# Kernel tuning notes

Hardware: AMD Instinct MI355X
Metric: run time of the kernel (lower is better)

The kernel has to match this reference:

```python
import jax, jax.numpy as jnp
import numpy as np

# Fixed causal graph: 32 endo nodes, each with a private 16-dim exogenous parent.
# Nodes 0..3 are roots (no endo parents); node i>=4 has endo parents {i-4..i-1}.
N_NODES = 32
ENDO = 16      # endogenous features per node
EXO = 16       # exogenous features per node
HID = 64       # hidden width (module default hidden_features=[64,64])
N_ROOTS = 4
N_PAR = 4      # endo parents for non-root nodes
IN_ROOT = EXO                      # 16
IN_INNER = N_PAR * ENDO + EXO      # 80
BATCH = 32768


def _init(key, shape, fan_in):
    return jax.random.normal(key, shape, jnp.float32) * (1.0 / np.sqrt(fan_in))


def setup_inputs() -> dict:
    key = jax.random.key(0)
    ks = jax.random.split(key, 13)
    n_in = N_NODES - N_ROOTS
    return {
        "u": jax.random.normal(ks[0], (BATCH, N_NODES * EXO), jnp.float32),
        # stacked root MLPs: [n_roots, in, out]
        "w_r1": _init(ks[1], (N_ROOTS, IN_ROOT, HID), IN_ROOT),
        "b_r1": jnp.zeros((N_ROOTS, HID), jnp.float32),
        "w_r2": _init(ks[2], (N_ROOTS, HID, HID), HID),
        "b_r2": jnp.zeros((N_ROOTS, HID), jnp.float32),
        "w_r3": _init(ks[3], (N_ROOTS, HID, ENDO), HID),
        "b_r3": jnp.zeros((N_ROOTS, ENDO), jnp.float32),
        # stacked inner MLPs: [n_inner, in, out]
        "w_i1": _init(ks[4], (n_in, IN_INNER, HID), IN_INNER),
        "b_i1": jnp.zeros((n_in, HID), jnp.float32),
        "w_i2": _init(ks[5], (n_in, HID, HID), HID),
        "b_i2": jnp.zeros((n_in, HID), jnp.float32),
        "w_i3": _init(ks[6], (n_in, HID, ENDO), HID),
        "b_i3": jnp.zeros((n_in, ENDO), jnp.float32),
    }


def _mlp(x, w1, b1, w2, b2, w3, b3):
    h = jax.nn.relu(x @ w1 + b1)
    h = jax.nn.relu(h @ w2 + b2)
    return h @ w3 + b3


def reference(u, w_r1, b_r1, w_r2, b_r2, w_r3, b_r3,
              w_i1, b_i1, w_i2, b_i2, w_i3, b_i3):
    B = u.shape[0]
    U = u.reshape(B, N_NODES, EXO)  # per-node exogenous inputs
    # Root nodes: no endo parents, vectorized over the 4 roots.
    h = jax.nn.relu(jnp.einsum("bni,nio->bno", U[:, :N_ROOTS], w_r1) + b_r1)
    h = jax.nn.relu(jnp.einsum("bnh,nho->bno", h, w_r2) + b_r2)
    root_v = jnp.einsum("bnh,nhd->bnd", h, w_r3) + b_r3  # [B, 4, ENDO]
    V = [root_v[:, i] for i in range(N_ROOTS)]
    # Non-root nodes in topological order: gather thresholded parents -> MLP.
    for i in range(N_ROOTS, N_NODES):
        j = i - N_ROOTS
        parents = jnp.concatenate(
            [(V[p] > 0.5).astype(u.dtype) for p in range(i - N_PAR, i)], axis=-1)
        inp = jnp.concatenate([parents, U[:, i]], axis=-1)  # [B, 80]
        V.append(_mlp(inp, w_i1[j], b_i1[j], w_i2[j], b_i2[j], w_i3[j], b_i3[j]))
    # forward() uses soft=True, T/W_T/W_E=None -> E is the raw logits, batched.
    return jnp.concatenate(V, axis=-1)  # [B, N_NODES*ENDO]
```

## Files before the change

kernel.cpp:

```cpp
#include <hip/hip_runtime.h>


#define BT 64

typedef __attribute__((ext_vector_type(8))) short bf16x8;
typedef __attribute__((ext_vector_type(4))) float f32x4;
#define MFMA16 __builtin_amdgcn_mfma_f32_16x16x32_bf16

#define NODE_STRIDE 33792
#define W1_SPLIT    6144
#define W2_OFF      18432
#define W2_SPLIT    4096
#define W3_OFF      30720
#define W3_SPLIT    1024

__device__ inline unsigned short bf16_rne(float x) {
    unsigned u = __float_as_uint(x);
    u += 0x7fffu + ((u >> 16) & 1u);
    return (unsigned short)(u >> 16);
}
__device__ inline float bf16_tof(unsigned short h) {
    return __uint_as_float(((unsigned)h) << 16);
}
__device__ inline void split3(float x, unsigned short& h, unsigned short& m,
                              unsigned short& l) {
    h = bf16_rne(x);
    float r = x - bf16_tof(h);
    m = bf16_rne(r);
    float r2 = r - bf16_tof(m);
    l = bf16_rne(r2);
}

#define PER_NODE_ITEMS (64 * 96 + 64 * 64 + 16 * 64)

__global__ void prep_weights(const float* __restrict__ w_r1,
                             const float* __restrict__ w_r2,
                             const float* __restrict__ w_r3,
                             const float* __restrict__ w_i1,
                             const float* __restrict__ w_i2,
                             const float* __restrict__ w_i3,
                             unsigned short* __restrict__ ws) {
    int tid = blockIdx.x * 256 + threadIdx.x;
    if (tid >= 32 * PER_NODE_ITEMS) return;
    int node = tid / PER_NODE_ITEMS;
    int r = tid - node * PER_NODE_ITEMS;
    int off, stride;
    float wv = 0.0f;
    if (r < 6144) {
        int n = r / 96, k = r - n * 96;
        if (k < 64) {
            wv = (node >= 4) ? w_i1[((node - 4) * 80 + k) * 64 + n] : 0.0f;
        } else if (k < 80) {
            wv = (node < 4) ? w_r1[(node * 16 + (k - 64)) * 64 + n]
                            : w_i1[((node - 4) * 80 + k) * 64 + n];
        }
        off = n * 96 + k; stride = W1_SPLIT;
    } else if (r < 10240) {
        int r2 = r - 6144;
        int n = r2 >> 6, k = r2 & 63;
        wv = (node < 4) ? w_r2[(node * 64 + k) * 64 + n]
                        : w_i2[((node - 4) * 64 + k) * 64 + n];
        off = W2_OFF + n * 64 + k; stride = W2_SPLIT;
    } else {
        int r3 = r - 10240;
        int n = r3 >> 6, k = r3 & 63;
        wv = (node < 4) ? w_r3[(node * 64 + k) * 16 + n]
                        : w_i3[((node - 4) * 64 + k) * 16 + n];
        off = W3_OFF + n * 64 + k; stride = W3_SPLIT;
    }
    unsigned short h, m, l;
    split3(wv, h, m, l);
    unsigned short* base = ws + node * NODE_STRIDE;
    base[off] = h;
    base[off + stride] = m;
    base[off + 2 * stride] = l;
}

__global__ __launch_bounds__(256, 2) void ncm_mfma(
    const float* __restrict__ u,
    const unsigned short* __restrict__ ws,
    const float* __restrict__ b_r1, const float* __restrict__ b_r2,
    const float* __restrict__ b_r3, const float* __restrict__ b_i1,
    const float* __restrict__ b_i2, const float* __restrict__ b_i3,
    float* __restrict__ out)
{
    __shared__ __align__(16) unsigned short ring[4][64][24];
    __shared__ __align__(16) unsigned short xu[3][64][32];
    __shared__ __align__(16) unsigned short h1s[3][64][72];
    __shared__ __align__(16) unsigned short h2s[3][64][72];

    const int tid = threadIdx.x;
    const int l   = tid & 63;
    const int w   = tid >> 6;
    const int lr  = l & 15;
    const int lq  = l >> 4;

    for (int z = tid; z < 4 * 64 * 24; z += 256) ((unsigned short*)ring)[z] = 0;
    for (int z = tid; z < 3 * 64 * 32; z += 256) ((unsigned short*)xu)[z] = 0;

    const long eg = (long)blockIdx.x * BT;
    const float* u_blk = u + eg * 512;
    const int n1 = 16 * w + lr;

    for (int i = 0; i < 32; ++i) {
        __syncthreads();

        float4 uv = *(const float4*)(u_blk + (long)l * 512 + i * 16 + w * 4);
        {
            unsigned short h0, m0, l0, h1, m1, l1, h2, m2, l2, h3, m3, l3;
            split3(uv.x, h0, m0, l0); split3(uv.y, h1, m1, l1);
            split3(uv.z, h2, m2, l2); split3(uv.w, h3, m3, l3);
            ushort4 vh = make_ushort4(h0, h1, h2, h3);
            ushort4 vm = make_ushort4(m0, m1, m2, m3);
            ushort4 vl = make_ushort4(l0, l1, l2, l3);
            *(ushort4*)&xu[0][l][4 * w] = vh;
            *(ushort4*)&xu[1][l][4 * w] = vm;
            *(ushort4*)&xu[2][l][4 * w] = vl;
        }
        __syncthreads();

        const unsigned short* Wn = ws + i * NODE_STRIDE;

        f32x4 acc[4] = {{0,0,0,0},{0,0,0,0},{0,0,0,0},{0,0,0,0}};
        {
            if (i >= 4) {
                #pragma unroll
                for (int k0 = 0; k0 < 64; k0 += 32) {
                    const int f = k0 + lq * 8;
                    const int slot = (i + (f >> 4)) & 3;
                    bf16x8 wb0 = *(const bf16x8*)(Wn + 0 * W1_SPLIT + n1 * 96 + f);
                    bf16x8 wb1 = *(const bf16x8*)(Wn + 1 * W1_SPLIT + n1 * 96 + f);
                    bf16x8 wb2 = *(const bf16x8*)(Wn + 2 * W1_SPLIT + n1 * 96 + f);
                    #pragma unroll
                    for (int m = 0; m < 4; ++m) {
                        bf16x8 ab = *(const bf16x8*)&ring[slot][m * 16 + lr][f & 15];
                        acc[m] = MFMA16(ab, wb0, acc[m], 0, 0, 0);
                        acc[m] = MFMA16(ab, wb1, acc[m], 0, 0, 0);
                        acc[m] = MFMA16(ab, wb2, acc[m], 0, 0, 0);
                    }
                }
            }
            {
                const int f = lq * 8;
                bf16x8 wb0 = *(const bf16x8*)(Wn + 0 * W1_SPLIT + n1 * 96 + 64 + f);
                bf16x8 wb1 = *(const bf16x8*)(Wn + 1 * W1_SPLIT + n1 * 96 + 64 + f);
                bf16x8 wb2 = *(const bf16x8*)(Wn + 2 * W1_SPLIT + n1 * 96 + 64 + f);
                #pragma unroll
                for (int m = 0; m < 4; ++m) {
                    const int e = m * 16 + lr;
                    bf16x8 a0 = *(const bf16x8*)&xu[0][e][f];
                    bf16x8 a1 = *(const bf16x8*)&xu[1][e][f];
                    bf16x8 a2 = *(const bf16x8*)&xu[2][e][f];
                    acc[m] = MFMA16(a0, wb0, acc[m], 0, 0, 0);
                    acc[m] = MFMA16(a0, wb1, acc[m], 0, 0, 0);
                    acc[m] = MFMA16(a0, wb2, acc[m], 0, 0, 0);
                    acc[m] = MFMA16(a1, wb0, acc[m], 0, 0, 0);
                    acc[m] = MFMA16(a1, wb1, acc[m], 0, 0, 0);
                    acc[m] = MFMA16(a1, wb2, acc[m], 0, 0, 0);
                    acc[m] = MFMA16(a2, wb0, acc[m], 0, 0, 0);
                    acc[m] = MFMA16(a2, wb1, acc[m], 0, 0, 0);
                }
            }
            const float b1 = (i < 4) ? b_r1[i * 64 + n1] : b_i1[(i - 4) * 64 + n1];
            #pragma unroll
            for (int m = 0; m < 4; ++m) {
                #pragma unroll
                for (int r = 0; r < 4; ++r) {
                    const int e = m * 16 + lq * 4 + r;
                    float v = fmaxf(acc[m][r] + b1, 0.0f);
                    unsigned short sh, sm, sl;
                    split3(v, sh, sm, sl);
                    h1s[0][e][n1] = sh; h1s[1][e][n1] = sm; h1s[2][e][n1] = sl;
                }
            }
        }
        __syncthreads();

        {
            #pragma unroll
            for (int m = 0; m < 4; ++m) acc[m] = (f32x4){0,0,0,0};
            const unsigned short* W2 = Wn + W2_OFF;
            #pragma unroll
            for (int k0 = 0; k0 < 64; k0 += 32) {
                const int f = k0 + lq * 8;
                bf16x8 wb0 = *(const bf16x8*)(W2 + 0 * W2_SPLIT + n1 * 64 + f);
                bf16x8 wb1 = *(const bf16x8*)(W2 + 1 * W2_SPLIT + n1 * 64 + f);
                bf16x8 wb2 = *(const bf16x8*)(W2 + 2 * W2_SPLIT + n1 * 64 + f);
                #pragma unroll
                for (int m = 0; m < 4; ++m) {
                    const int e = m * 16 + lr;
                    bf16x8 a0 = *(const bf16x8*)&h1s[0][e][f];
                    bf16x8 a1 = *(const bf16x8*)&h1s[1][e][f];
                    bf16x8 a2 = *(const bf16x8*)&h1s[2][e][f];
                    acc[m] = MFMA16(a0, wb0, acc[m], 0, 0, 0);
                    acc[m] = MFMA16(a0, wb1, acc[m], 0, 0, 0);
                    acc[m] = MFMA16(a0, wb2, acc[m], 0, 0, 0);
                    acc[m] = MFMA16(a1, wb0, acc[m], 0, 0, 0);
                    acc[m] = MFMA16(a1, wb1, acc[m], 0, 0, 0);
                    acc[m] = MFMA16(a1, wb2, acc[m], 0, 0, 0);
                    acc[m] = MFMA16(a2, wb0, acc[m], 0, 0, 0);
                    acc[m] = MFMA16(a2, wb1, acc[m], 0, 0, 0);
                }
            }
            const float b2 = (i < 4) ? b_r2[i * 64 + n1] : b_i2[(i - 4) * 64 + n1];
            #pragma unroll
            for (int m = 0; m < 4; ++m) {
                #pragma unroll
                for (int r = 0; r < 4; ++r) {
                    const int e = m * 16 + lq * 4 + r;
                    float v = fmaxf(acc[m][r] + b2, 0.0f);
                    unsigned short sh, sm, sl;
                    split3(v, sh, sm, sl);
                    h2s[0][e][n1] = sh; h2s[1][e][n1] = sm; h2s[2][e][n1] = sl;
                }
            }
        }
        __syncthreads();

        {
            f32x4 c3 = {0,0,0,0};
            const unsigned short* W3 = Wn + W3_OFF;
            #pragma unroll
            for (int k0 = 0; k0 < 64; k0 += 32) {
                const int f = k0 + lq * 8;
                bf16x8 wb0 = *(const bf16x8*)(W3 + 0 * W3_SPLIT + lr * 64 + f);
                bf16x8 wb1 = *(const bf16x8*)(W3 + 1 * W3_SPLIT + lr * 64 + f);
                bf16x8 wb2 = *(const bf16x8*)(W3 + 2 * W3_SPLIT + lr * 64 + f);
                const int e = 16 * w + lr;
                bf16x8 a0 = *(const bf16x8*)&h2s[0][e][f];
                bf16x8 a1 = *(const bf16x8*)&h2s[1][e][f];
                bf16x8 a2 = *(const bf16x8*)&h2s[2][e][f];
                c3 = MFMA16(a0, wb0, c3, 0, 0, 0);
                c3 = MFMA16(a0, wb1, c3, 0, 0, 0);
                c3 = MFMA16(a0, wb2, c3, 0, 0, 0);
                c3 = MFMA16(a1, wb0, c3, 0, 0, 0);
                c3 = MFMA16(a1, wb1, c3, 0, 0, 0);
                c3 = MFMA16(a1, wb2, c3, 0, 0, 0);
                c3 = MFMA16(a2, wb0, c3, 0, 0, 0);
                c3 = MFMA16(a2, wb1, c3, 0, 0, 0);
            }
            const float b3 = (i < 4) ? b_r3[i * 16 + lr] : b_i3[(i - 4) * 16 + lr];
            const int slot = i & 3;
            #pragma unroll
            for (int r = 0; r < 4; ++r) {
                const int e = 16 * w + lq * 4 + r;
                float v = c3[r] + b3;
                out[(eg + e) * 512 + i * 16 + lr] = v;
                ring[slot][e][lr] = (v > 0.5f) ? (unsigned short)0x3F80 : (unsigned short)0;
            }
        }
    }
}

extern "C" void kernel_launch(void* const* d_in, const int* in_sizes, int n_in,
                              void* d_out, int out_size, void* d_ws, size_t ws_size,
                              hipStream_t stream) {
    const float* u    = (const float*)d_in[0];
    const float* w_r1 = (const float*)d_in[1];
    const float* b_r1 = (const float*)d_in[2];
    const float* w_r2 = (const float*)d_in[3];
    const float* b_r2 = (const float*)d_in[4];
    const float* w_r3 = (const float*)d_in[5];
    const float* b_r3 = (const float*)d_in[6];
    const float* w_i1 = (const float*)d_in[7];
    const float* b_i1 = (const float*)d_in[8];
    const float* w_i2 = (const float*)d_in[9];
    const float* b_i2 = (const float*)d_in[10];
    const float* w_i3 = (const float*)d_in[11];
    const float* b_i3 = (const float*)d_in[12];
    float* out = (float*)d_out;
    unsigned short* ws = (unsigned short*)d_ws;

    prep_weights<<<dim3((32 * PER_NODE_ITEMS) / 256), dim3(256), 0, stream>>>(
        w_r1, w_r2, w_r3, w_i1, w_i2, w_i3, ws);

    ncm_mfma<<<dim3(512), dim3(256), 0, stream>>>(
        u, ws, b_r1, b_r2, b_r3, b_i1, b_i2, b_i3, out);
}
```

Measured before the change: 335.6 us.

## Give each wave its own 16-row batch slice to drop block barriers

Work is redistributed so each wave owns 16 batch rows end to end for all 32 nodes, with per-wave shared buffers. Block-wide __syncthreads become wave barriers. Operands are swapped so MFMA outputs are feature-major per row, which enables vectorized bias loads, ushort4 stores and float4 output writes. The cost is that each wave now loads the full weight set itself, so weight traffic from L1/L2 per wave rises about fourfold.

```diff
diff --git a/kernel.cpp b/kernel.cpp
--- a/kernel.cpp
+++ b/kernel.cpp
@@ -84,10 +84,10 @@
     const float* __restrict__ b_i2, const float* __restrict__ b_i3,
     float* __restrict__ out)
 {
-    __shared__ __align__(16) unsigned short ring[4][64][24];
-    __shared__ __align__(16) unsigned short xu[3][64][32];
-    __shared__ __align__(16) unsigned short h1s[3][64][72];
-    __shared__ __align__(16) unsigned short h2s[3][64][72];
+    __shared__ __align__(16) unsigned short ring[4][4][16][24];
+    __shared__ __align__(16) unsigned short xu[4][3][16][32];
+    __shared__ __align__(16) unsigned short h1s[4][3][16][72];
+    __shared__ __align__(16) unsigned short h2s[4][3][16][72];
 
     const int tid = threadIdx.x;
     const int l   = tid & 63;
@@ -95,160 +95,174 @@
     const int lr  = l & 15;
     const int lq  = l >> 4;
 
-    for (int z = tid; z < 4 * 64 * 24; z += 256) ((unsigned short*)ring)[z] = 0;
-    for (int z = tid; z < 3 * 64 * 32; z += 256) ((unsigned short*)xu)[z] = 0;
-
-    const long eg = (long)blockIdx.x * BT;
-    const float* u_blk = u + eg * 512;
-    const int n1 = 16 * w + lr;
+    for (int z = l; z < 4 * 16 * 24; z += 64) ((unsigned short*)ring[w])[z] = 0;
+    for (int z = l; z < 3 * 16 * 32; z += 64) ((unsigned short*)xu[w])[z] = 0;
+    __builtin_amdgcn_wave_barrier();
+
+    const long eg   = (long)blockIdx.x * BT;
+    const long erow = eg + w * 16 + lr;
+    const float* u_row   = u   + erow * 512;
+    float*       out_row = out + erow * 512;
 
     for (int i = 0; i < 32; ++i) {
-        __syncthreads();
-
-        float4 uv = *(const float4*)(u_blk + (long)l * 512 + i * 16 + w * 4);
-        {
+        const unsigned short* Wn = ws + i * NODE_STRIDE;
+
+        {
+            float4 uv = *(const float4*)(u_row + i * 16 + lq * 4);
             unsigned short h0, m0, l0, h1, m1, l1, h2, m2, l2, h3, m3, l3;
             split3(uv.x, h0, m0, l0); split3(uv.y, h1, m1, l1);
             split3(uv.z, h2, m2, l2); split3(uv.w, h3, m3, l3);
-            ushort4 vh = make_ushort4(h0, h1, h2, h3);
-            ushort4 vm = make_ushort4(m0, m1, m2, m3);
-            ushort4 vl = make_ushort4(l0, l1, l2, l3);
-            *(ushort4*)&xu[0][l][4 * w] = vh;
-            *(ushort4*)&xu[1][l][4 * w] = vm;
-            *(ushort4*)&xu[2][l][4 * w] = vl;
-        }
-        __syncthreads();
-
-        const unsigned short* Wn = ws + i * NODE_STRIDE;
+            *(ushort4*)&xu[w][0][lr][lq * 4] = make_ushort4(h0, h1, h2, h3);
+            *(ushort4*)&xu[w][1][lr][lq * 4] = make_ushort4(m0, m1, m2, m3);
+            *(ushort4*)&xu[w][2][lr][lq * 4] = make_ushort4(l0, l1, l2, l3);
+        }
+        __builtin_amdgcn_wave_barrier();
 
         f32x4 acc[4] = {{0,0,0,0},{0,0,0,0},{0,0,0,0},{0,0,0,0}};
-        {
-            if (i >= 4) {
-                #pragma unroll
-                for (int k0 = 0; k0 < 64; k0 += 32) {
-                    const int f = k0 + lq * 8;
-                    const int slot = (i + (f >> 4)) & 3;
-                    bf16x8 wb0 = *(const bf16x8*)(Wn + 0 * W1_SPLIT + n1 * 96 + f);
-                    bf16x8 wb1 = *(const bf16x8*)(Wn + 1 * W1_SPLIT + n1 * 96 + f);
-                    bf16x8 wb2 = *(const bf16x8*)(Wn + 2 * W1_SPLIT + n1 * 96 + f);
-                    #pragma unroll
-                    for (int m = 0; m < 4; ++m) {
-                        bf16x8 ab = *(const bf16x8*)&ring[slot][m * 16 + lr][f & 15];
-                        acc[m] = MFMA16(ab, wb0, acc[m], 0, 0, 0);
-                        acc[m] = MFMA16(ab, wb1, acc[m], 0, 0, 0);
-                        acc[m] = MFMA16(ab, wb2, acc[m], 0, 0, 0);
-                    }
-                }
-            }
-            {
-                const int f = lq * 8;
-                bf16x8 wb0 = *(const bf16x8*)(Wn + 0 * W1_SPLIT + n1 * 96 + 64 + f);
-                bf16x8 wb1 = *(const bf16x8*)(Wn + 1 * W1_SPLIT + n1 * 96 + 64 + f);
-                bf16x8 wb2 = *(const bf16x8*)(Wn + 2 * W1_SPLIT + n1 * 96 + 64 + f);
-                #pragma unroll
-                for (int m = 0; m < 4; ++m) {
-                    const int e = m * 16 + lr;
-                    bf16x8 a0 = *(const bf16x8*)&xu[0][e][f];
-                    bf16x8 a1 = *(const bf16x8*)&xu[1][e][f];
-                    bf16x8 a2 = *(const bf16x8*)&xu[2][e][f];
-                    acc[m] = MFMA16(a0, wb0, acc[m], 0, 0, 0);
-                    acc[m] = MFMA16(a0, wb1, acc[m], 0, 0, 0);
-                    acc[m] = MFMA16(a0, wb2, acc[m], 0, 0, 0);
-                    acc[m] = MFMA16(a1, wb0, acc[m], 0, 0, 0);
-                    acc[m] = MFMA16(a1, wb1, acc[m], 0, 0, 0);
-                    acc[m] = MFMA16(a1, wb2, acc[m], 0, 0, 0);
-                    acc[m] = MFMA16(a2, wb0, acc[m], 0, 0, 0);
-                    acc[m] = MFMA16(a2, wb1, acc[m], 0, 0, 0);
-                }
-            }
-            const float b1 = (i < 4) ? b_r1[i * 64 + n1] : b_i1[(i - 4) * 64 + n1];
-            #pragma unroll
-            for (int m = 0; m < 4; ++m) {
-                #pragma unroll
-                for (int r = 0; r < 4; ++r) {
-                    const int e = m * 16 + lq * 4 + r;
-                    float v = fmaxf(acc[m][r] + b1, 0.0f);
-                    unsigned short sh, sm, sl;
-                    split3(v, sh, sm, sl);
-                    h1s[0][e][n1] = sh; h1s[1][e][n1] = sm; h1s[2][e][n1] = sl;
-                }
-            }
-        }
-        __syncthreads();
-
-        {
-            #pragma unroll
-            for (int m = 0; m < 4; ++m) acc[m] = (f32x4){0,0,0,0};
-            const unsigned short* W2 = Wn + W2_OFF;
+
+        if (i >= 4) {
             #pragma unroll
             for (int k0 = 0; k0 < 64; k0 += 32) {
                 const int f = k0 + lq * 8;
-                bf16x8 wb0 = *(const bf16x8*)(W2 + 0 * W2_SPLIT + n1 * 64 + f);
-                bf16x8 wb1 = *(const bf16x8*)(W2 + 1 * W2_SPLIT + n1 * 64 + f);
-                bf16x8 wb2 = *(const bf16x8*)(W2 + 2 * W2_SPLIT + n1 * 64 + f);
+                const int slot = (i + (f >> 4)) & 3;
+                bf16x8 ab = *(const bf16x8*)&ring[w][slot][lr][f & 15];
                 #pragma unroll
-                for (int m = 0; m < 4; ++m) {
-                    const int e = m * 16 + lr;
-                    bf16x8 a0 = *(const bf16x8*)&h1s[0][e][f];
-                    bf16x8 a1 = *(const bf16x8*)&h1s[1][e][f];
-                    bf16x8 a2 = *(const bf16x8*)&h1s[2][e][f];
-                    acc[m] = MFMA16(a0, wb0, acc[m], 0, 0, 0);
-                    acc[m] = MFMA16(a0, wb1, acc[m], 0, 0, 0);
-                    acc[m] = MFMA16(a0, wb2, acc[m], 0, 0, 0);
-                    acc[m] = MFMA16(a1, wb0, acc[m], 0, 0, 0);
-                    acc[m] = MFMA16(a1, wb1, acc[m], 0, 0, 0);
-                    acc[m] = MFMA16(a1, wb2, acc[m], 0, 0, 0);
-                    acc[m] = MFMA16(a2, wb0, acc[m], 0, 0, 0);
-                    acc[m] = MFMA16(a2, wb1, acc[m], 0, 0, 0);
+                for (int ft = 0; ft < 4; ++ft) {
+                    const unsigned short* wp = Wn + (ft * 16 + lr) * 96 + f;
+                    bf16x8 wb0 = *(const bf16x8*)(wp);
+                    bf16x8 wb1 = *(const bf16x8*)(wp + W1_SPLIT);
+                    bf16x8 wb2 = *(const bf16x8*)(wp + 2 * W1_SPLIT);
+                    acc[ft] = MFMA16(wb0, ab, acc[ft], 0, 0, 0);
+                    acc[ft] = MFMA16(wb1, ab, acc[ft], 0, 0, 0);
+                    acc[ft] = MFMA16(wb2, ab, acc[ft], 0, 0, 0);
                 }
             }
-            const float b2 = (i < 4) ? b_r2[i * 64 + n1] : b_i2[(i - 4) * 64 + n1];
-            #pragma unroll
-            for (int m = 0; m < 4; ++m) {
-                #pragma unroll
-                for (int r = 0; r < 4; ++r) {
-                    const int e = m * 16 + lq * 4 + r;
-                    float v = fmaxf(acc[m][r] + b2, 0.0f);
-                    unsigned short sh, sm, sl;
-                    split3(v, sh, sm, sl);
-                    h2s[0][e][n1] = sh; h2s[1][e][n1] = sm; h2s[2][e][n1] = sl;
-                }
-            }
-        }
-        __syncthreads();
-
-        {
-            f32x4 c3 = {0,0,0,0};
-            const unsigned short* W3 = Wn + W3_OFF;
+        }
+        {
+            const int f = lq * 8;
+            bf16x8 a0 = *(const bf16x8*)&xu[w][0][lr][f];
+            bf16x8 a1 = *(const bf16x8*)&xu[w][1][lr][f];
+            bf16x8 a2 = *(const bf16x8*)&xu[w][2][lr][f];
+            #pragma unroll
+            for (int ft = 0; ft < 4; ++ft) {
+                const unsigned short* wp = Wn + (ft * 16 + lr) * 96 + 64 + f;
+                bf16x8 wb0 = *(const bf16x8*)(wp);
+                bf16x8 wb1 = *(const bf16x8*)(wp + W1_SPLIT);
+                bf16x8 wb2 = *(const bf16x8*)(wp + 2 * W1_SPLIT);
+                acc[ft] = MFMA16(wb0, a0, acc[ft], 0, 0, 0);
+                acc[ft] = MFMA16(wb1, a0, acc[ft], 0, 0, 0);
+                acc[ft] = MFMA16(wb2, a0, acc[ft], 0, 0, 0);
+                acc[ft] = MFMA16(wb0, a1, acc[ft], 0, 0, 0);
+                acc[ft] = MFMA16(wb1, a1, acc[ft], 0, 0, 0);
+                acc[ft] = MFMA16(wb2, a1, acc[ft], 0, 0, 0);
+                acc[ft] = MFMA16(wb0, a2, acc[ft], 0, 0, 0);
+                acc[ft] = MFMA16(wb1, a2, acc[ft], 0, 0, 0);
+            }
+        }
+        {
+            const float* B1 = (i < 4) ? (b_r1 + i * 64) : (b_i1 + (i - 4) * 64);
+            #pragma unroll
+            for (int ft = 0; ft < 4; ++ft) {
+                float4 bv = *(const float4*)(B1 + ft * 16 + lq * 4);
+                float v0 = fmaxf(acc[ft][0] + bv.x, 0.0f);
+                float v1 = fmaxf(acc[ft][1] + bv.y, 0.0f);
+                float v2 = fmaxf(acc[ft][2] + bv.z, 0.0f);
+                float v3 = fmaxf(acc[ft][3] + bv.w, 0.0f);
+                unsigned short h0, m0, l0, h1, m1, l1, h2, m2, l2, h3, m3, l3;
+                split3(v0, h0, m0, l0); split3(v1, h1, m1, l1);
+                split3(v2, h2, m2, l2); split3(v3, h3, m3, l3);
+                const int o = ft * 16 + lq * 4;
+                *(ushort4*)&h1s[w][0][lr][o] = make_ushort4(h0, h1, h2, h3);
+                *(ushort4*)&h1s[w][1][lr][o] = make_ushort4(m0, m1, m2, m3);
+                *(ushort4*)&h1s[w][2][lr][o] = make_ushort4(l0, l1, l2, l3);
+            }
+        }
+        __builtin_amdgcn_wave_barrier();
+
+        #pragma unroll
+        for (int ft = 0; ft < 4; ++ft) acc[ft] = (f32x4){0, 0, 0, 0};
+        {
+            const unsigned short* W2 = Wn + W2_OFF;
             #pragma unroll
             for (int k0 = 0; k0 < 64; k0 += 32) {
                 const int f = k0 + lq * 8;
-                bf16x8 wb0 = *(const bf16x8*)(W3 + 0 * W3_SPLIT + lr * 64 + f);
-                bf16x8 wb1 = *(const bf16x8*)(W3 + 1 * W3_SPLIT + lr * 64 + f);
-                bf16x8 wb2 = *(const bf16x8*)(W3 + 2 * W3_SPLIT + lr * 64 + f);
-                const int e = 16 * w + lr;
-                bf16x8 a0 = *(const bf16x8*)&h2s[0][e][f];
-                bf16x8 a1 = *(const bf16x8*)&h2s[1][e][f];
-                bf16x8 a2 = *(const bf16x8*)&h2s[2][e][f];
-                c3 = MFMA16(a0, wb0, c3, 0, 0, 0);
-                c3 = MFMA16(a0, wb1, c3, 0, 0, 0);
-                c3 = MFMA16(a0, wb2, c3, 0, 0, 0);
-                c3 = MFMA16(a1, wb0, c3, 0, 0, 0);
-                c3 = MFMA16(a1, wb1, c3, 0, 0, 0);
-                c3 = MFMA16(a1, wb2, c3, 0, 0, 0);
-                c3 = MFMA16(a2, wb0, c3, 0, 0, 0);
-                c3 = MFMA16(a2, wb1, c3, 0, 0, 0);
-            }
-            const float b3 = (i < 4) ? b_r3[i * 16 + lr] : b_i3[(i - 4) * 16 + lr];
+                bf16x8 a0 = *(const bf16x8*)&h1s[w][0][lr][f];
+                bf16x8 a1 = *(const bf16x8*)&h1s[w][1][lr][f];
+                bf16x8 a2 = *(const bf16x8*)&h1s[w][2][lr][f];
+                #pragma unroll
+                for (int ft = 0; ft < 4; ++ft) {
+                    const unsigned short* wp = W2 + (ft * 16 + lr) * 64 + f;
+                    bf16x8 wb0 = *(const bf16x8*)(wp);
+                    bf16x8 wb1 = *(const bf16x8*)(wp + W2_SPLIT);
+                    bf16x8 wb2 = *(const bf16x8*)(wp + 2 * W2_SPLIT);
+                    acc[ft] = MFMA16(wb0, a0, acc[ft], 0, 0, 0);
+                    acc[ft] = MFMA16(wb1, a0, acc[ft], 0, 0, 0);
+                    acc[ft] = MFMA16(wb2, a0, acc[ft], 0, 0, 0);
+                    acc[ft] = MFMA16(wb0, a1, acc[ft], 0, 0, 0);
+                    acc[ft] = MFMA16(wb1, a1, acc[ft], 0, 0, 0);
+                    acc[ft] = MFMA16(wb2, a1, acc[ft], 0, 0, 0);
+                    acc[ft] = MFMA16(wb0, a2, acc[ft], 0, 0, 0);
+                    acc[ft] = MFMA16(wb1, a2, acc[ft], 0, 0, 0);
+                }
+            }
+        }
+        {
+            const float* B2 = (i < 4) ? (b_r2 + i * 64) : (b_i2 + (i - 4) * 64);
+            #pragma unroll
+            for (int ft = 0; ft < 4; ++ft) {
+                float4 bv = *(const float4*)(B2 + ft * 16 + lq * 4);
+                float v0 = fmaxf(acc[ft][0] + bv.x, 0.0f);
+                float v1 = fmaxf(acc[ft][1] + bv.y, 0.0f);
+                float v2 = fmaxf(acc[ft][2] + bv.z, 0.0f);
+                float v3 = fmaxf(acc[ft][3] + bv.w, 0.0f);
+                unsigned short h0, m0, l0, h1, m1, l1, h2, m2, l2, h3, m3, l3;
+                split3(v0, h0, m0, l0); split3(v1, h1, m1, l1);
+                split3(v2, h2, m2, l2); split3(v3, h3, m3, l3);
+                const int o = ft * 16 + lq * 4;
+                *(ushort4*)&h2s[w][0][lr][o] = make_ushort4(h0, h1, h2, h3);
+                *(ushort4*)&h2s[w][1][lr][o] = make_ushort4(m0, m1, m2, m3);
+                *(ushort4*)&h2s[w][2][lr][o] = make_ushort4(l0, l1, l2, l3);
+            }
+        }
+        __builtin_amdgcn_wave_barrier();
+
+        {
+            f32x4 c3 = {0, 0, 0, 0};
+            const unsigned short* W3 = Wn + W3_OFF;
+            #pragma unroll
+            for (int k0 = 0; k0 < 64; k0 += 32) {
+                const int f = k0 + lq * 8;
+                bf16x8 a0 = *(const bf16x8*)&h2s[w][0][lr][f];
+                bf16x8 a1 = *(const bf16x8*)&h2s[w][1][lr][f];
+                bf16x8 a2 = *(const bf16x8*)&h2s[w][2][lr][f];
+                const unsigned short* wp = W3 + lr * 64 + f;
+                bf16x8 wb0 = *(const bf16x8*)(wp);
+                bf16x8 wb1 = *(const bf16x8*)(wp + W3_SPLIT);
+                bf16x8 wb2 = *(const bf16x8*)(wp + 2 * W3_SPLIT);
+                c3 = MFMA16(wb0, a0, c3, 0, 0, 0);
+                c3 = MFMA16(wb1, a0, c3, 0, 0, 0);
+                c3 = MFMA16(wb2, a0, c3, 0, 0, 0);
+                c3 = MFMA16(wb0, a1, c3, 0, 0, 0);
+                c3 = MFMA16(wb1, a1, c3, 0, 0, 0);
+                c3 = MFMA16(wb2, a1, c3, 0, 0, 0);
+                c3 = MFMA16(wb0, a2, c3, 0, 0, 0);
+                c3 = MFMA16(wb1, a2, c3, 0, 0, 0);
+            }
+            const float* B3 = (i < 4) ? (b_r3 + i * 16) : (b_i3 + (i - 4) * 16);
+            float4 bv = *(const float4*)(B3 + lq * 4);
+            float v0 = c3[0] + bv.x;
+            float v1 = c3[1] + bv.y;
+            float v2 = c3[2] + bv.z;
+            float v3 = c3[3] + bv.w;
+            *(float4*)(out_row + i * 16 + lq * 4) = make_float4(v0, v1, v2, v3);
             const int slot = i & 3;
-            #pragma unroll
-            for (int r = 0; r < 4; ++r) {
-                const int e = 16 * w + lq * 4 + r;
-                float v = c3[r] + b3;
-                out[(eg + e) * 512 + i * 16 + lr] = v;
-                ring[slot][e][lr] = (v > 0.5f) ? (unsigned short)0x3F80 : (unsigned short)0;
-            }
-        }
+            *(ushort4*)&ring[w][slot][lr][lq * 4] = make_ushort4(
+                v0 > 0.5f ? (unsigned short)0x3F80 : (unsigned short)0,
+                v1 > 0.5f ? (unsigned short)0x3F80 : (unsigned short)0,
+                v2 > 0.5f ? (unsigned short)0x3F80 : (unsigned short)0,
+                v3 > 0.5f ? (unsigned short)0x3F80 : (unsigned short)0);
+        }
+        __builtin_amdgcn_wave_barrier();
     }
 }
 
```

Result: slower. 490.3 us (+46.1%).
